# Kernel optimization log

Measured on AMD Instinct MI355X. Metric: run time of the kernel, lower is better.

The kernel has to match this reference:

```python
import jax, jax.numpy as jnp
import numpy as np

HEADS = 8
DIM_HEAD = 64
EPS = 1e-5  # PyTorch InstanceNorm default eps


def _instance_norm_lastdim(t):
    # PyTorch InstanceNorm1d on (b*h, n, d) with affine=False normalizes over
    # the last (spatial) axis d per (sample, token), biased variance.
    mu = jnp.mean(t, axis=-1, keepdims=True)
    var = jnp.mean(jnp.square(t - mu), axis=-1, keepdims=True)
    return (t - mu) / jnp.sqrt(var + EPS)


def setup_inputs() -> dict:
    key = jax.random.key(0)
    k1, k2, k3, k4, k5 = jax.random.split(key, 5)
    b, n1, n2, dim = 4, 8192, 8192, 256
    inner = HEADS * DIM_HEAD  # 512
    return {
        "x": jax.random.normal(k1, (b, n1, dim), jnp.float32),
        "z": jax.random.normal(k2, (b, n2, dim), jnp.float32),
        "Wq": jax.random.normal(k3, (dim, inner), jnp.float32) * 0.02,
        "Wkv": jax.random.normal(k4, (dim, 2 * inner), jnp.float32) * 0.02,
        "Wout": jax.random.normal(k5, (inner, dim), jnp.float32) * 0.02,
        "bout": jnp.zeros((dim,), jnp.float32),
    }


def reference(x, z, Wq, Wkv, Wout, bout):
    b, n1, _ = x.shape
    n2 = z.shape[1]
    h, d = HEADS, DIM_HEAD

    q = x @ Wq                     # [b, n1, h*d]
    kv = z @ Wkv                   # [b, n2, 2*h*d]
    k, v = jnp.split(kv, 2, axis=-1)

    q = q.reshape(b, n1, h, d).transpose(0, 2, 1, 3)  # b h n1 d
    k = k.reshape(b, n2, h, d).transpose(0, 2, 1, 3)  # b h n2 d
    v = v.reshape(b, n2, h, d).transpose(0, 2, 1, 3)  # b h n2 d

    # galerkin: normalize k and v
    k = _instance_norm_lastdim(k)
    v = _instance_norm_lastdim(v)

    # linear-attention kernel trick: (k^T v) then q @ dots, scaled by 1/n2
    dots = jnp.einsum('bhnd,bhne->bhde', k, v)          # [b, h, d, d]
    out = jnp.einsum('bhnd,bhde->bhne', q, dots) / n2   # [b, h, n1, d]

    out = out.transpose(0, 2, 1, 3).reshape(b, n1, h * d)
    return out @ Wout + bout
```

## Files before the change

kernel.cpp:

```cpp
#include <hip/hip_runtime.h>
#include <cstddef>

#define NB    4
#define NTOK  8192
#define DIMX  256
#define NH    8
#define HD    64
#define INNER 512
#define SPLIT 32
#define EPS   1e-5f

typedef __attribute__((ext_vector_type(8))) short short8;
typedef __attribute__((ext_vector_type(4))) float f32x4;

__device__ __forceinline__ unsigned short f2bf(float f) {
  union { float f; unsigned u; } v; v.f = f;
  unsigned r = v.u + 0x7fffu + ((v.u >> 16) & 1u);
  return (unsigned short)(r >> 16);
}

__global__ __launch_bounds__(256) void k_pre(
    const float* __restrict__ z, unsigned short* __restrict__ zb,
    const float* __restrict__ Wkv, unsigned short* __restrict__ wkvT)
{
  __shared__ unsigned short t[64][68];
  if (blockIdx.x < 2048) {
    const size_t i = ((size_t)blockIdx.x * 256 + threadIdx.x) * 16;
    float4 a0 = *(const float4*)(z + i);
    float4 a1 = *(const float4*)(z + i + 4);
    float4 a2 = *(const float4*)(z + i + 8);
    float4 a3 = *(const float4*)(z + i + 12);
    short8 p0, p1;
    p0[0] = (short)f2bf(a0.x); p0[1] = (short)f2bf(a0.y);
    p0[2] = (short)f2bf(a0.z); p0[3] = (short)f2bf(a0.w);
    p0[4] = (short)f2bf(a1.x); p0[5] = (short)f2bf(a1.y);
    p0[6] = (short)f2bf(a1.z); p0[7] = (short)f2bf(a1.w);
    p1[0] = (short)f2bf(a2.x); p1[1] = (short)f2bf(a2.y);
    p1[2] = (short)f2bf(a2.z); p1[3] = (short)f2bf(a2.w);
    p1[4] = (short)f2bf(a3.x); p1[5] = (short)f2bf(a3.y);
    p1[6] = (short)f2bf(a3.z); p1[7] = (short)f2bf(a3.w);
    *(short8*)(zb + i) = p0;
    *(short8*)(zb + i + 8) = p1;
  } else {
    const int tid = threadIdx.x;
    const int bb = blockIdx.x - 2048;
    const int r0 = (bb & 3) * 64;
    const int c0 = (bb >> 2) * 64;
    const int r = tid >> 2;
    const int c4 = (tid & 3) * 16;
#pragma unroll
    for (int j = 0; j < 4; ++j) {
      float4 v = *(const float4*)(Wkv + (size_t)(r0 + r) * (2 * INNER) + c0 + c4 + j * 4);
      t[r][c4 + j * 4 + 0] = f2bf(v.x);
      t[r][c4 + j * 4 + 1] = f2bf(v.y);
      t[r][c4 + j * 4 + 2] = f2bf(v.z);
      t[r][c4 + j * 4 + 3] = f2bf(v.w);
    }
    __syncthreads();
    const int cc = tid >> 2;
    const int rr4 = (tid & 3) * 16;
    short8 o0, o1;
#pragma unroll
    for (int i = 0; i < 8; ++i) o0[i] = (short)t[rr4 + i][cc];
#pragma unroll
    for (int i = 0; i < 8; ++i) o1[i] = (short)t[rr4 + 8 + i][cc];
    unsigned short* dst = wkvT + (size_t)(c0 + cc) * DIMX + r0 + rr4;
    *(short8*)(dst) = o0;
    *(short8*)(dst + 8) = o1;
  }
}

__global__ __launch_bounds__(256) void k_dots_mfma(
    const unsigned short* __restrict__ zb, const unsigned short* __restrict__ wkvT,
    float* __restrict__ partial)
{
  const int tid  = threadIdx.x;
  const int lane = tid & 63;
  const int w    = tid >> 6;
  const int l15  = lane & 15;
  const int lg   = lane >> 4;

  const int bid = blockIdx.x;
  const int s = bid & (SPLIT - 1);
  const int h = (bid >> 5) & (NH - 1);
  const int b = bid >> 8;

  __shared__ unsigned short zs[32][268];
  __shared__ unsigned short kv2[128][36];
  __shared__ float sum1[4][32];
  __shared__ float sum2[4][32];

  short8 awf[2][8];
#pragma unroll
  for (int mf = 0; mf < 2; ++mf) {
    const int dim = w * 32 + mf * 16 + l15;
    const int gd = (dim < HD) ? (h * HD + dim) : (INNER + h * HD + (dim - HD));
    const unsigned short* base = wkvT + (size_t)gd * DIMX + lg * 8;
#pragma unroll
    for (int kk = 0; kk < 8; ++kk)
      awf[mf][kk] = *(const short8*)(base + kk * 32);
  }

  f32x4 dacc[4];
#pragma unroll
  for (int nf = 0; nf < 4; ++nf) dacc[nf] = (f32x4){0.f, 0.f, 0.f, 0.f};

  const int zr = tid >> 3;
  const int zc = (tid & 7) * 32;
  const unsigned short* zbase = zb + ((size_t)b * NTOK + s * 256 + zr) * DIMX + zc;

  {
    short8 pre[4];
#pragma unroll
    for (int j = 0; j < 4; ++j) pre[j] = *(const short8*)(zbase + j * 8);
#pragma unroll
    for (int j = 0; j < 4; ++j) *(short8*)&zs[zr][zc + j * 8] = pre[j];
  }
  __syncthreads();

  for (int tile = 0; tile < 8; ++tile) {
    short8 pre[4];
    if (tile < 7) {
      const unsigned short* src = zbase + (size_t)(tile + 1) * 32 * DIMX;
#pragma unroll
      for (int j = 0; j < 4; ++j) pre[j] = *(const short8*)(src + j * 8);
    }

    f32x4 acc[2][2];
#pragma unroll
    for (int mf = 0; mf < 2; ++mf)
#pragma unroll
      for (int nf = 0; nf < 2; ++nf) acc[mf][nf] = (f32x4){0.f, 0.f, 0.f, 0.f};

#pragma unroll
    for (int kk = 0; kk < 8; ++kk) {
      short8 bfr[2];
#pragma unroll
      for (int nf = 0; nf < 2; ++nf)
        bfr[nf] = *(const short8*)&zs[nf * 16 + l15][kk * 32 + lg * 8];
#pragma unroll
      for (int mf = 0; mf < 2; ++mf)
#pragma unroll
        for (int nf = 0; nf < 2; ++nf)
          acc[mf][nf] = __builtin_amdgcn_mfma_f32_16x16x32_bf16(
              awf[mf][kk], bfr[nf], acc[mf][nf], 0, 0, 0);
    }

    float s1[2], s2[2];
#pragma unroll
    for (int nf = 0; nf < 2; ++nf) {
      float a = 0.f, q = 0.f;
#pragma unroll
      for (int mf = 0; mf < 2; ++mf)
#pragma unroll
        for (int r = 0; r < 4; ++r) {
          float v = acc[mf][nf][r];
          a += v; q += v * v;
        }
      a += __shfl_xor(a, 16); a += __shfl_xor(a, 32);
      q += __shfl_xor(q, 16); q += __shfl_xor(q, 32);
      s1[nf] = a; s2[nf] = q;
    }
    if (lg == 0) {
#pragma unroll
      for (int nf = 0; nf < 2; ++nf) {
        sum1[w][nf * 16 + l15] = s1[nf];
        sum2[w][nf * 16 + l15] = s2[nf];
      }
    }
    __syncthreads();

    if (tile < 7) {
#pragma unroll
      for (int j = 0; j < 4; ++j) *(short8*)&zs[zr][zc + j * 8] = pre[j];
    }

    if (w < 2) {
      const int p = w ^ 1;
      float mu[2];
#pragma unroll
      for (int nf = 0; nf < 2; ++nf)
        mu[nf] = (s1[nf] + sum1[p][nf * 16 + l15]) * (1.f / 64.f);
#pragma unroll
      for (int mf = 0; mf < 2; ++mf)
#pragma unroll
        for (int nf = 0; nf < 2; ++nf)
#pragma unroll
          for (int r = 0; r < 4; ++r)
            kv2[w * 32 + mf * 16 + lg * 4 + r][nf * 16 + l15] =
                f2bf(acc[mf][nf][r] - mu[nf]);
    } else {
      const int p = w ^ 1;
      float sc[2], ms[2];
#pragma unroll
      for (int nf = 0; nf < 2; ++nf) {
        const int tok = nf * 16 + l15;
        const float t1v = s1[nf] + sum1[p][tok];
        const float t2v = s2[nf] + sum2[p][tok];
        const float muv = t1v * (1.f / 64.f);
        const float rv = rsqrtf(t2v * (1.f / 64.f) - muv * muv + EPS);
        const float t1k = sum1[0][tok] + sum1[1][tok];
        const float t2k = sum2[0][tok] + sum2[1][tok];
        const float muk = t1k * (1.f / 64.f);
        const float rk = rsqrtf(t2k * (1.f / 64.f) - muk * muk + EPS);
        sc[nf] = rk * rv;
        ms[nf] = muv * sc[nf];
      }
#pragma unroll
      for (int mf = 0; mf < 2; ++mf)
#pragma unroll
        for (int nf = 0; nf < 2; ++nf)
#pragma unroll
          for (int r = 0; r < 4; ++r)
            kv2[(w - 2) * 32 + 64 + mf * 16 + lg * 4 + r][nf * 16 + l15] =
                f2bf(fmaf(acc[mf][nf][r], sc[nf], -ms[nf]));
    }
    __syncthreads();

    {
      short8 a2 = *(const short8*)&kv2[w * 16 + l15][lg * 8];
#pragma unroll
      for (int nf = 0; nf < 4; ++nf) {
        short8 b2 = *(const short8*)&kv2[64 + nf * 16 + l15][lg * 8];
        dacc[nf] = __builtin_amdgcn_mfma_f32_16x16x32_bf16(a2, b2, dacc[nf], 0, 0, 0);
      }
    }
  }

  float* pb = partial + ((size_t)((b * NH + h) * SPLIT + s)) * 4096;
#pragma unroll
  for (int nf = 0; nf < 4; ++nf)
#pragma unroll
    for (int r = 0; r < 4; ++r)
      pb[(w * 16 + lg * 4 + r) * 64 + nf * 16 + l15] = dacc[nf][r];
}

__global__ __launch_bounds__(256) void k_reduce(
    const float* __restrict__ partial, float* __restrict__ dots)
{
  const int idx = blockIdx.x * 256 + threadIdx.x;
  const int bh = idx >> 12;
  const int de = idx & 4095;
  const float* p = partial + (size_t)bh * SPLIT * 4096 + de;
  float s = 0.f;
#pragma unroll
  for (int i = 0; i < SPLIT; ++i) s += p[(size_t)i * 4096];
  dots[idx] = s * (1.f / (float)NTOK);
}

__global__ __launch_bounds__(256) void k_bdwout(
    const float* __restrict__ dots, const float* __restrict__ Wout,
    float* __restrict__ tmp)
{
  const int bid = blockIdx.x;
  const int b = bid >> 7;
  const int r4 = (bid & 127) * 4;
  const int h = r4 >> 6;
  const int c = threadIdx.x;
  const float* dr = dots + (size_t)(b * NH + h) * 4096 + (size_t)(r4 & 63) * 64;
  float a0 = 0.f, a1 = 0.f, a2 = 0.f, a3 = 0.f;
#pragma unroll 8
  for (int j = 0; j < 64; ++j) {
    const float wv = Wout[(size_t)(h * 64 + j) * DIMX + c];
    a0 += dr[j] * wv;
    a1 += dr[64 + j] * wv;
    a2 += dr[128 + j] * wv;
    a3 += dr[192 + j] * wv;
  }
  float* tb = tmp + ((size_t)b * INNER + r4) * DIMX + c;
  tb[0] = a0; tb[DIMX] = a1; tb[2 * DIMX] = a2; tb[3 * DIMX] = a3;
}

__global__ __launch_bounds__(256) void k_weff(
    const float* __restrict__ Wq, const float* __restrict__ tmp,
    unsigned short* __restrict__ weffT)
{
  const int bid = blockIdx.x;
  const int b = bid >> 6;
  const int r4 = (bid & 63) * 4;
  const int c = threadIdx.x;
  const float* tb = tmp + (size_t)b * INNER * DIMX + c;
  float a0 = 0.f, a1 = 0.f, a2 = 0.f, a3 = 0.f;
#pragma unroll 8
  for (int k = 0; k < INNER; ++k) {
    const float t = tb[(size_t)k * DIMX];
    a0 += Wq[(size_t)(r4 + 0) * INNER + k] * t;
    a1 += Wq[(size_t)(r4 + 1) * INNER + k] * t;
    a2 += Wq[(size_t)(r4 + 2) * INNER + k] * t;
    a3 += Wq[(size_t)(r4 + 3) * INNER + k] * t;
  }
  unsigned short* wb = weffT + ((size_t)b * DIMX + c) * DIMX + r4;
  wb[0] = f2bf(a0); wb[1] = f2bf(a1); wb[2] = f2bf(a2); wb[3] = f2bf(a3);
}

__global__ __launch_bounds__(256) void k_out_mfma(
    const float* __restrict__ x, const unsigned short* __restrict__ weffT,
    const float* __restrict__ bout, float* __restrict__ out)
{
  const int tid  = threadIdx.x;
  const int lane = tid & 63;
  const int w    = tid >> 6;
  const int l15  = lane & 15;
  const int lg   = lane >> 4;

  const int bid = blockIdx.x;
  const int mt = bid & 127;
  const int b  = bid >> 7;
  const int tok0 = mt * 64;

  __shared__ unsigned short wsl[2][256 * 36];

  short8 afr[8];
  {
    const float* xr = x + ((size_t)b * NTOK + tok0 + w * 16 + l15) * DIMX + lg * 8;
#pragma unroll
    for (int kk = 0; kk < 8; ++kk) {
      float4 xa = *(const float4*)(xr + kk * 32);
      float4 xb = *(const float4*)(xr + kk * 32 + 4);
      short8 a;
      a[0] = (short)f2bf(xa.x); a[1] = (short)f2bf(xa.y);
      a[2] = (short)f2bf(xa.z); a[3] = (short)f2bf(xa.w);
      a[4] = (short)f2bf(xb.x); a[5] = (short)f2bf(xb.y);
      a[6] = (short)f2bf(xb.z); a[7] = (short)f2bf(xb.w);
      afr[kk] = a;
    }
  }

  f32x4 acc[16];
#pragma unroll
  for (int nf = 0; nf < 16; ++nf) acc[nf] = (f32x4){0.f, 0.f, 0.f, 0.f};

  const unsigned short* wb = weffT + (size_t)b * DIMX * DIMX + (size_t)tid * DIMX;

  {
#pragma unroll
    for (int j = 0; j < 4; ++j) {
      short8 g = *(const short8*)(wb + j * 8);
      *(short8*)&wsl[0][tid * 36 + j * 8] = g;
    }
  }
  __syncthreads();

  for (int kk = 0; kk < 8; ++kk) {
    short8 g[4];
    if (kk < 7) {
#pragma unroll
      for (int j = 0; j < 4; ++j)
        g[j] = *(const short8*)(wb + (kk + 1) * 32 + j * 8);
    }
#pragma unroll
    for (int nf = 0; nf < 16; ++nf) {
      short8 b2 = *(const short8*)&wsl[kk & 1][(nf * 16 + l15) * 36 + lg * 8];
      acc[nf] = __builtin_amdgcn_mfma_f32_16x16x32_bf16(afr[kk], b2, acc[nf], 0, 0, 0);
    }
    if (kk < 7) {
#pragma unroll
      for (int j = 0; j < 4; ++j)
        *(short8*)&wsl[(kk + 1) & 1][tid * 36 + j * 8] = g[j];
    }
    __syncthreads();
  }

#pragma unroll
  for (int nf = 0; nf < 16; ++nf) {
    const float bias = bout[nf * 16 + l15];
#pragma unroll
    for (int r = 0; r < 4; ++r) {
      const int row = tok0 + w * 16 + lg * 4 + r;
      out[((size_t)b * NTOK + row) * DIMX + nf * 16 + l15] = acc[nf][r] + bias;
    }
  }
}

extern "C" void kernel_launch(void* const* d_in, const int* in_sizes, int n_in,
                              void* d_out, int out_size, void* d_ws, size_t ws_size,
                              hipStream_t stream) {
  const float* x    = (const float*)d_in[0];
  const float* z    = (const float*)d_in[1];
  const float* Wq   = (const float*)d_in[2];
  const float* Wkv  = (const float*)d_in[3];
  const float* Wout = (const float*)d_in[4];
  const float* bout = (const float*)d_in[5];
  float* out = (float*)d_out;

  float* ws   = (float*)d_ws;
  float* dots = ws;
  float* tmp  = dots + (size_t)NB * NH * 4096;
  unsigned short* wkvT  = (unsigned short*)(tmp + (size_t)NB * INNER * DIMX);
  unsigned short* weffT = wkvT + (size_t)(2 * INNER) * DIMX;

  unsigned short* zbf = (unsigned short*)d_out;
  float* partial = (float*)((char*)d_out + ((size_t)16 << 20));

  k_pre<<<2112, 256, 0, stream>>>(z, zbf, Wkv, wkvT);
  k_dots_mfma<<<NB * NH * SPLIT, 256, 0, stream>>>(zbf, wkvT, partial);
  k_reduce<<<512, 256, 0, stream>>>(partial, dots);
  k_bdwout<<<NB * 128, 256, 0, stream>>>(dots, Wout, tmp);
  k_weff<<<NB * 64, 256, 0, stream>>>(Wq, tmp, weffT);
  k_out_mfma<<<NB * 128, 256, 0, stream>>>(x, weffT, bout, out);
}
```

Baseline: 101.7 us.

## Remap warps so each owns full head dim, double-buffer LDS to drop barrier

Each warp now computes all 64 dims of either k or v for 16 tokens, so the instance-norm mean and variance reduce within a warp via shuffles. The cross-warp partial-sum exchange through shared memory and its extra barrier are gone. The z tile and kv2 staging buffers are double-buffered so each tile needs one __syncthreads instead of two. This raises register use (awf grows to 4x8 short8 fragments) and doubles LDS, with launch_bounds(256,2) added to keep occupancy.

```diff
diff --git a/kernel.cpp b/kernel.cpp
--- a/kernel.cpp
+++ b/kernel.cpp
@@ -70,13 +70,15 @@
   }
 }
 
-__global__ __launch_bounds__(256) void k_dots_mfma(
+__global__ __launch_bounds__(256, 2) void k_dots_mfma(
     const unsigned short* __restrict__ zb, const unsigned short* __restrict__ wkvT,
     float* __restrict__ partial)
 {
   const int tid  = threadIdx.x;
   const int lane = tid & 63;
   const int w    = tid >> 6;
+  const int wm   = w >> 1;
+  const int wn   = w & 1;
   const int l15  = lane & 15;
   const int lg   = lane >> 4;
 
@@ -85,15 +87,13 @@
   const int h = (bid >> 5) & (NH - 1);
   const int b = bid >> 8;
 
-  __shared__ unsigned short zs[32][268];
-  __shared__ unsigned short kv2[128][36];
-  __shared__ float sum1[4][32];
-  __shared__ float sum2[4][32];
-
-  short8 awf[2][8];
-#pragma unroll
-  for (int mf = 0; mf < 2; ++mf) {
-    const int dim = w * 32 + mf * 16 + l15;
+  __shared__ unsigned short zs[2][32][268];
+  __shared__ unsigned short kv2[2][128][36];
+
+  short8 awf[4][8];
+#pragma unroll
+  for (int mf = 0; mf < 4; ++mf) {
+    const int dim = wm * 64 + mf * 16 + l15;
     const int gd = (dim < HD) ? (h * HD + dim) : (INNER + h * HD + (dim - HD));
     const unsigned short* base = wkvT + (size_t)gd * DIMX + lg * 8;
 #pragma unroll
@@ -114,10 +114,11 @@
 #pragma unroll
     for (int j = 0; j < 4; ++j) pre[j] = *(const short8*)(zbase + j * 8);
 #pragma unroll
-    for (int j = 0; j < 4; ++j) *(short8*)&zs[zr][zc + j * 8] = pre[j];
+    for (int j = 0; j < 4; ++j) *(short8*)&zs[0][zr][zc + j * 8] = pre[j];
   }
   __syncthreads();
 
+  int cur = 0;
   for (int tile = 0; tile < 8; ++tile) {
     short8 pre[4];
     if (tile < 7) {
@@ -126,105 +127,54 @@
       for (int j = 0; j < 4; ++j) pre[j] = *(const short8*)(src + j * 8);
     }
 
-    f32x4 acc[2][2];
-#pragma unroll
-    for (int mf = 0; mf < 2; ++mf)
-#pragma unroll
-      for (int nf = 0; nf < 2; ++nf) acc[mf][nf] = (f32x4){0.f, 0.f, 0.f, 0.f};
+    f32x4 acc[4];
+#pragma unroll
+    for (int mf = 0; mf < 4; ++mf) acc[mf] = (f32x4){0.f, 0.f, 0.f, 0.f};
 
 #pragma unroll
     for (int kk = 0; kk < 8; ++kk) {
-      short8 bfr[2];
-#pragma unroll
-      for (int nf = 0; nf < 2; ++nf)
-        bfr[nf] = *(const short8*)&zs[nf * 16 + l15][kk * 32 + lg * 8];
-#pragma unroll
-      for (int mf = 0; mf < 2; ++mf)
-#pragma unroll
-        for (int nf = 0; nf < 2; ++nf)
-          acc[mf][nf] = __builtin_amdgcn_mfma_f32_16x16x32_bf16(
-              awf[mf][kk], bfr[nf], acc[mf][nf], 0, 0, 0);
-    }
-
-    float s1[2], s2[2];
-#pragma unroll
-    for (int nf = 0; nf < 2; ++nf) {
-      float a = 0.f, q = 0.f;
-#pragma unroll
-      for (int mf = 0; mf < 2; ++mf)
-#pragma unroll
-        for (int r = 0; r < 4; ++r) {
-          float v = acc[mf][nf][r];
-          a += v; q += v * v;
-        }
-      a += __shfl_xor(a, 16); a += __shfl_xor(a, 32);
-      q += __shfl_xor(q, 16); q += __shfl_xor(q, 32);
-      s1[nf] = a; s2[nf] = q;
-    }
-    if (lg == 0) {
-#pragma unroll
-      for (int nf = 0; nf < 2; ++nf) {
-        sum1[w][nf * 16 + l15] = s1[nf];
-        sum2[w][nf * 16 + l15] = s2[nf];
+      short8 bfr = *(const short8*)&zs[cur][wn * 16 + l15][kk * 32 + lg * 8];
+#pragma unroll
+      for (int mf = 0; mf < 4; ++mf)
+        acc[mf] = __builtin_amdgcn_mfma_f32_16x16x32_bf16(
+            awf[mf][kk], bfr, acc[mf], 0, 0, 0);
+    }
+
+    float a = 0.f, q = 0.f;
+#pragma unroll
+    for (int mf = 0; mf < 4; ++mf)
+#pragma unroll
+      for (int r = 0; r < 4; ++r) {
+        float v = acc[mf][r];
+        a += v; q += v * v;
       }
+    a += __shfl_xor(a, 16); a += __shfl_xor(a, 32);
+    q += __shfl_xor(q, 16); q += __shfl_xor(q, 32);
+    const float mu = a * (1.f / 64.f);
+    const float rs = rsqrtf(q * (1.f / 64.f) - mu * mu + EPS);
+
+#pragma unroll
+    for (int mf = 0; mf < 4; ++mf)
+#pragma unroll
+      for (int r = 0; r < 4; ++r)
+        kv2[cur][wm * 64 + mf * 16 + lg * 4 + r][wn * 16 + l15] =
+            f2bf((acc[mf][r] - mu) * rs);
+
+    if (tile < 7) {
+#pragma unroll
+      for (int j = 0; j < 4; ++j) *(short8*)&zs[cur ^ 1][zr][zc + j * 8] = pre[j];
     }
     __syncthreads();
 
-    if (tile < 7) {
-#pragma unroll
-      for (int j = 0; j < 4; ++j) *(short8*)&zs[zr][zc + j * 8] = pre[j];
-    }
-
-    if (w < 2) {
-      const int p = w ^ 1;
-      float mu[2];
-#pragma unroll
-      for (int nf = 0; nf < 2; ++nf)
-        mu[nf] = (s1[nf] + sum1[p][nf * 16 + l15]) * (1.f / 64.f);
-#pragma unroll
-      for (int mf = 0; mf < 2; ++mf)
-#pragma unroll
-        for (int nf = 0; nf < 2; ++nf)
-#pragma unroll
-          for (int r = 0; r < 4; ++r)
-            kv2[w * 32 + mf * 16 + lg * 4 + r][nf * 16 + l15] =
-                f2bf(acc[mf][nf][r] - mu[nf]);
-    } else {
-      const int p = w ^ 1;
-      float sc[2], ms[2];
-#pragma unroll
-      for (int nf = 0; nf < 2; ++nf) {
-        const int tok = nf * 16 + l15;
-        const float t1v = s1[nf] + sum1[p][tok];
-        const float t2v = s2[nf] + sum2[p][tok];
-        const float muv = t1v * (1.f / 64.f);
-        const float rv = rsqrtf(t2v * (1.f / 64.f) - muv * muv + EPS);
-        const float t1k = sum1[0][tok] + sum1[1][tok];
-        const float t2k = sum2[0][tok] + sum2[1][tok];
-        const float muk = t1k * (1.f / 64.f);
-        const float rk = rsqrtf(t2k * (1.f / 64.f) - muk * muk + EPS);
-        sc[nf] = rk * rv;
-        ms[nf] = muv * sc[nf];
-      }
-#pragma unroll
-      for (int mf = 0; mf < 2; ++mf)
-#pragma unroll
-        for (int nf = 0; nf < 2; ++nf)
-#pragma unroll
-          for (int r = 0; r < 4; ++r)
-            kv2[(w - 2) * 32 + 64 + mf * 16 + lg * 4 + r][nf * 16 + l15] =
-                f2bf(fmaf(acc[mf][nf][r], sc[nf], -ms[nf]));
-    }
-    __syncthreads();
-
     {
-      short8 a2 = *(const short8*)&kv2[w * 16 + l15][lg * 8];
+      short8 a2 = *(const short8*)&kv2[cur][w * 16 + l15][lg * 8];
 #pragma unroll
       for (int nf = 0; nf < 4; ++nf) {
-        short8 b2 = *(const short8*)&kv2[64 + nf * 16 + l15][lg * 8];
+        short8 b2 = *(const short8*)&kv2[cur][64 + nf * 16 + l15][lg * 8];
         dacc[nf] = __builtin_amdgcn_mfma_f32_16x16x32_bf16(a2, b2, dacc[nf], 0, 0, 0);
       }
     }
+    cur ^= 1;
   }
 
   float* pb = partial + ((size_t)((b * NH + h) * SPLIT + s)) * 4096;
```

Measured after the change: 103.3 us. Within noise of the previous version (+1.6%).
